# Performance work log

Hardware: AMD Instinct MI355X
Metric: run time of the kernel (lower is better)

## Reference

```python
import jax, jax.numpy as jnp
import numpy as np

B, S, D = 4, 1024, 2048
N_HEADS, N_KV_HEADS = 32, 8
HEAD_DIM = D // N_HEADS          # 64
HALF = HEAD_DIM // 2             # 32
N_REP = N_HEADS // N_KV_HEADS    # 4


def setup_inputs() -> dict:
    key = jax.random.key(0)
    ks = jax.random.split(key, 6)
    # rotary tables: freqs_cis = exp(i * t * theta^( -2j/d )), real cos/sin halves
    inv_freq = 1.0 / (10000.0 ** (np.arange(0, HEAD_DIM, 2, dtype=np.float32) / HEAD_DIM))
    t = np.arange(S, dtype=np.float32)
    angles = np.outer(t, inv_freq)  # [S, HALF]
    return {
        "x": jax.random.normal(ks[0], (B, S, D), dtype=jnp.float32),
        "pos_cos": jnp.asarray(np.cos(angles), dtype=jnp.float32),
        "pos_sin": jnp.asarray(np.sin(angles), dtype=jnp.float32),
        "wq": jax.random.normal(ks[1], (D, N_HEADS * HEAD_DIM), dtype=jnp.float32) / np.sqrt(D),
        "wk": jax.random.normal(ks[2], (D, N_KV_HEADS * HEAD_DIM), dtype=jnp.float32) / np.sqrt(D),
        "wv": jax.random.normal(ks[3], (D, N_KV_HEADS * HEAD_DIM), dtype=jnp.float32) / np.sqrt(D),
        "wo": jax.random.normal(ks[4], (D, D), dtype=jnp.float32) / np.sqrt(D),
    }


def _apply_rotary(t, cos, sin):
    # t: [B, S, H, head_dim]; pairs of consecutive elements form complex numbers
    te = t[..., 0::2]  # real parts  [B,S,H,HALF]
    to = t[..., 1::2]  # imag parts
    c = cos[None, :, None, :]
    s = sin[None, :, None, :]
    re = te * c - to * s
    im = te * s + to * c
    return jnp.stack([re, im], axis=-1).reshape(t.shape)


def reference(x, pos_cos, pos_sin, wq, wk, wv, wo):
    b, s, d = x.shape
    xq = (x @ wq).reshape(b, s, N_HEADS, HEAD_DIM)
    xk = (x @ wk).reshape(b, s, N_KV_HEADS, HEAD_DIM)
    xv = (x @ wv).reshape(b, s, N_KV_HEADS, HEAD_DIM)
    xq = _apply_rotary(xq, pos_cos, pos_sin)
    xk = _apply_rotary(xk, pos_cos, pos_sin)
    # GQA: repeat kv heads (kv head h -> heads h*N_REP..h*N_REP+N_REP-1)
    xk = jnp.repeat(xk, N_REP, axis=2)
    xv = jnp.repeat(xv, N_REP, axis=2)
    scores = jnp.einsum("bqhd,bkhd->bhqk", xq, xk) / np.sqrt(HEAD_DIM).astype(np.float32)
    causal = jnp.triu(jnp.ones((s, s), dtype=bool), k=1)
    scores = jnp.where(causal[None, None], jnp.float32(-jnp.inf), scores)
    attn = jax.nn.softmax(scores.astype(jnp.float32), axis=-1).astype(x.dtype)
    out = jnp.einsum("bhqk,bkhd->bqhd", attn, xv).reshape(b, s, d)
    return out @ wo
```

## Files before the change

### kernel.cpp

```cpp
#include <hip/hip_runtime.h>
#include <hip/hip_bf16.h>


typedef __bf16 bf16x8 __attribute__((ext_vector_type(8)));
typedef float  f32x4  __attribute__((ext_vector_type(4)));

#define DEV static __device__ __forceinline__

DEV unsigned short f2bf(float f) {
  __hip_bfloat16 h = __float2bfloat16(f);
  unsigned short u;
  __builtin_memcpy(&u, &h, 2);
  return u;
}
DEV float bf2f(unsigned short u) {
  unsigned int ui = ((unsigned int)u) << 16;
  float f;
  __builtin_memcpy(&f, &ui, 4);
  return f;
}

typedef const unsigned int __attribute__((address_space(1)))* as1_u32cp;
typedef unsigned int __attribute__((address_space(3)))* as3_u32p;

DEV void load16_lds(const unsigned short* g, unsigned short* l) {
  __builtin_amdgcn_global_load_lds((as1_u32cp)(unsigned long long)g,
                                   (as3_u32p)(unsigned int)(unsigned long long)l,
                                   16, 0, 0);
}

DEV f32x4 mfma16x16(bf16x8 a, bf16x8 b, f32x4 c) {
  return __builtin_amdgcn_mfma_f32_16x16x32_bf16(a, b, c, 0, 0, 0);
}

__global__ __launch_bounds__(256) void k_convert_x(const float* __restrict__ x,
                                                   unsigned short* __restrict__ xb, int n) {
  int i = (blockIdx.x * 256 + threadIdx.x) * 4;
  if (i < n) {
    float4 v = *(const float4*)(x + i);
    ushort4 o;
    o.x = f2bf(v.x); o.y = f2bf(v.y); o.z = f2bf(v.z); o.w = f2bf(v.w);
    *(ushort4*)(xb + i) = o;
  }
}

__global__ __launch_bounds__(256) void k_transpose_w(const float* __restrict__ src,
                                                     unsigned short* __restrict__ dst, int N) {
  __shared__ float t[32][33];
  const int n0 = blockIdx.x * 32, k0 = blockIdx.y * 32;
  const int tx = threadIdx.x & 31, ty = threadIdx.x >> 5;
#pragma unroll
  for (int i = 0; i < 4; i++) {
    int k = k0 + ty + i * 8;
    t[ty + i * 8][tx] = src[(size_t)k * N + n0 + tx];
  }
  __syncthreads();
#pragma unroll
  for (int i = 0; i < 4; i++) {
    int n = n0 + ty + i * 8;
    dst[(size_t)n * 2048 + k0 + tx] = f2bf(t[tx][ty + i * 8]);
  }
}

template <int OUTF32, int BN, int WM, int WN>
__global__ __launch_bounds__(512) void k_gemm8(const unsigned short* __restrict__ A,
                                               const unsigned short* __restrict__ Bt,
                                               void* __restrict__ Cp, int M, int N, int K) {
  constexpr int BM = 256;
  constexpr int FM = BM / WM / 16;
  constexpr int FN = BN / WN / 16;
  constexpr int LA = BM * 4 / 512;
  constexpr int LB = BN * 4 / 512;
  constexpr int LH = LA + LB;
  __shared__ __align__(16) unsigned short As[4][BM * 32];
  __shared__ __align__(16) unsigned short Bs[4][BN * 32];

  const int nbx = N / BN;
  const int nwg = gridDim.x;
  int wg = blockIdx.x;
  wg = (wg & 7) * (nwg >> 3) + (wg >> 3);
  const int bx = wg % nbx, by = wg / nbx;
  const int m0 = by << 8, n0 = bx * BN;
  const int tid = threadIdx.x;
  const int lane = tid & 63, wid = tid >> 6;
  const int wm = wid / WN, wn = wid % WN;
  const int l15 = lane & 15, kg = lane >> 4;
  const int H = K >> 5;
  const int NT = K >> 6;

  auto stageA = [&](int h, int i) {
    const int u = i * 512 + tid;
    const int row = u >> 2, sl = u & 3;
    const int gc = ((sl ^ ((row >> 1) & 3)) << 3);
    load16_lds(&A[(size_t)(m0 + row) * K + (h << 5) + gc],
               &As[h & 3][(i * 512 + (tid & ~63)) * 8]);
  };
  auto stageB = [&](int h, int i) {
    const int u = i * 512 + tid;
    const int row = u >> 2, sl = u & 3;
    const int gc = ((sl ^ ((row >> 1) & 3)) << 3);
    load16_lds(&Bt[(size_t)(n0 + row) * K + (h << 5) + gc],
               &Bs[h & 3][(i * 512 + (tid & ~63)) * 8]);
  };
  auto lda = [&](int s, int r) {
    return *(const bf16x8*)&As[s][r * 32 + ((kg ^ ((r >> 1) & 3)) << 3)];
  };
  auto ldb = [&](int s, int r) {
    return *(const bf16x8*)&Bs[s][r * 32 + ((kg ^ ((r >> 1) & 3)) << 3)];
  };

#define VMCNT_C2(c)                                                   \
  if ((c) == 2)      asm volatile("s_waitcnt vmcnt(%0)" ::"n"(2 * LH) : "memory"); \
  else if ((c) == 1) asm volatile("s_waitcnt vmcnt(%0)" ::"n"(LH) : "memory");     \
  else               asm volatile("s_waitcnt vmcnt(0)" ::: "memory");

  const int rowA0 = wm * (BM / WM) + l15;
  const int rowB0 = wn * (BN / WN) + l15;

  bf16x8 af[FM / 2], bf[FN];
  f32x4 acc[FM][FN] = {};

#pragma unroll
  for (int h = 0; h < 3; h++) {
    stageA(h, 0); stageA(h, 1);
    stageB(h, 0); if (LB > 1) stageB(h, 1);
  }
  asm volatile("s_waitcnt vmcnt(%0)" ::"n"(2 * LH) : "memory");
  __builtin_amdgcn_s_barrier();

  for (int t = 0; t < NT; t++) {
    const int s0 = (2 * t) & 3, s1 = (2 * t + 1) & 3;
    const int h3 = 2 * t + 3, h4 = 2 * t + 4;
    const bool v2 = (2 * t + 2) < H, v3 = h3 < H, v4 = h4 < H;

#pragma unroll
    for (int f = 0; f < FM / 2; f++) af[f] = lda(s0, rowA0 + f * 16);
#pragma unroll
    for (int g = 0; g < FN; g++) bf[g] = ldb(s0, rowB0 + g * 16);
    if (v3) { stageA(h3, 0); stageA(h3, 1); }
    __builtin_amdgcn_s_barrier();
    __builtin_amdgcn_s_setprio(1);
#pragma unroll
    for (int f = 0; f < FM / 2; f++)
#pragma unroll
      for (int g = 0; g < FN; g++) acc[f][g] = mfma16x16(af[f], bf[g], acc[f][g]);
    __builtin_amdgcn_s_setprio(0);

#pragma unroll
    for (int f = 0; f < FM / 2; f++) af[f] = lda(s0, rowA0 + (FM / 2 + f) * 16);
    if (v3) { stageB(h3, 0); if (LB > 1) stageB(h3, 1); }
    __builtin_amdgcn_s_barrier();
    __builtin_amdgcn_s_setprio(1);
#pragma unroll
    for (int f = 0; f < FM / 2; f++)
#pragma unroll
      for (int g = 0; g < FN; g++)
        acc[FM / 2 + f][g] = mfma16x16(af[f], bf[g], acc[FM / 2 + f][g]);
    __builtin_amdgcn_s_setprio(0);
    { const int c = (int)v2 + (int)v3; VMCNT_C2(c) }
    __builtin_amdgcn_s_barrier();

#pragma unroll
    for (int f = 0; f < FM / 2; f++) af[f] = lda(s1, rowA0 + f * 16);
#pragma unroll
    for (int g = 0; g < FN; g++) bf[g] = ldb(s1, rowB0 + g * 16);
    if (v4) { stageA(h4, 0); stageA(h4, 1); }
    __builtin_amdgcn_s_barrier();
    __builtin_amdgcn_s_setprio(1);
#pragma unroll
    for (int f = 0; f < FM / 2; f++)
#pragma unroll
      for (int g = 0; g < FN; g++) acc[f][g] = mfma16x16(af[f], bf[g], acc[f][g]);
    __builtin_amdgcn_s_setprio(0);

#pragma unroll
    for (int f = 0; f < FM / 2; f++) af[f] = lda(s1, rowA0 + (FM / 2 + f) * 16);
    if (v4) { stageB(h4, 0); if (LB > 1) stageB(h4, 1); }
    __builtin_amdgcn_s_barrier();
    __builtin_amdgcn_s_setprio(1);
#pragma unroll
    for (int f = 0; f < FM / 2; f++)
#pragma unroll
      for (int g = 0; g < FN; g++)
        acc[FM / 2 + f][g] = mfma16x16(af[f], bf[g], acc[FM / 2 + f][g]);
    __builtin_amdgcn_s_setprio(0);
    { const int c = (int)v3 + (int)v4; VMCNT_C2(c) }
    __builtin_amdgcn_s_barrier();
  }
#undef VMCNT_C2

  const int orow = m0 + wm * (BM / WM) + kg * 4;
#pragma unroll
  for (int fm = 0; fm < FM; fm++) {
#pragma unroll
    for (int fn = 0; fn < FN; fn++) {
      const int col = n0 + wn * (BN / WN) + fn * 16 + l15;
#pragma unroll
      for (int j = 0; j < 4; j++) {
        const size_t off = (size_t)(orow + fm * 16 + j) * N + col;
        if (OUTF32)
          ((float*)Cp)[off] = acc[fm][fn][j];
        else
          ((unsigned short*)Cp)[off] = f2bf(acc[fm][fn][j]);
      }
    }
  }
}

__global__ __launch_bounds__(256) void k_rope(unsigned short* __restrict__ qkv,
                                              const float* __restrict__ ctab,
                                              const float* __restrict__ stab) {
  const int idx = blockIdx.x * 256 + threadIdx.x;
  const int row = idx / 1280;
  const int r = idx - row * 1280;
  const int head = r >> 5, pair = r & 31;
  const int s = row & 1023;
  const int col = (head < 32) ? (head * 64 + pair * 2) : (2048 + (head - 32) * 64 + pair * 2);
  const float c = ctab[s * 32 + pair], sn = stab[s * 32 + pair];
  const size_t base = (size_t)row * 3072 + col;
  const float e = bf2f(qkv[base]), o = bf2f(qkv[base + 1]);
  qkv[base]     = f2bf(e * c - o * sn);
  qkv[base + 1] = f2bf(e * sn + o * c);
}

__global__ __launch_bounds__(256) void k_vt(const unsigned short* __restrict__ qkv,
                                            unsigned short* __restrict__ vt) {
  __shared__ unsigned short t[32][33];
  const int st0 = blockIdx.x * 32;
  const int d0 = blockIdx.y * 32;
  const int bkh = blockIdx.z;
  const int b = bkh >> 3, kh = bkh & 7;
  const int tx = threadIdx.x & 31, ty = threadIdx.x >> 5;
#pragma unroll
  for (int i = 0; i < 4; i++) {
    int s = st0 + ty + i * 8;
    t[ty + i * 8][tx] = qkv[(size_t)(b * 1024 + s) * 3072 + 2560 + kh * 64 + d0 + tx];
  }
  __syncthreads();
#pragma unroll
  for (int i = 0; i < 4; i++) {
    int d = d0 + ty + i * 8;
    vt[(size_t)(bkh * 64 + d) * 1024 + st0 + tx] = t[tx][ty + i * 8];
  }
}

__global__ __launch_bounds__(256) void k_attn(const unsigned short* __restrict__ qkv,
                                              const unsigned short* __restrict__ vt,
                                              unsigned short* __restrict__ ao) {
  __shared__ __align__(16) unsigned short Ks[2][64 * 64];
  __shared__ __align__(16) unsigned short Vs[2][64 * 64];
  __shared__ __align__(16) unsigned short P[4][16][72];

  const int bid = blockIdx.x;
  const int qt = 15 - (bid >> 7);
  const int hb = bid & 127;
  const int h = hb & 31, b = hb >> 5;
  const int q0 = qt << 6;
  const int wid = threadIdx.x >> 6, lane = threadIdx.x & 63;
  const int l15 = lane & 15, kg = lane >> 4;
  const int kh = h >> 2;
  const int qbase = b * 1024 + q0 + wid * 16;
  const int nt = qt + 1;
  const float NEGINF = -__builtin_inff();

  bf16x8 aq0, aq1;
  {
    const size_t qoff = (size_t)(qbase + l15) * 3072 + h * 64 + kg * 8;
    aq0 = *(const bf16x8*)&qkv[qoff];
    aq1 = *(const bf16x8*)&qkv[qoff + 32];
#pragma unroll
    for (int i = 0; i < 8; i++) {
      aq0[i] = (__bf16)((float)aq0[i] * 0.18033688011112042f);
      aq1[i] = (__bf16)((float)aq1[i] * 0.18033688011112042f);
    }
  }

  const int l8 = lane >> 3;
  const int colel = ((lane & 7) ^ l8) * 8;
  const size_t krowbase = (size_t)(b * 1024) * 3072 + 2048 + kh * 64 + colel;
  const size_t vrowbase = (size_t)((b * 8 + kh) * 64) * 1024 + colel;

#pragma unroll
  for (int i = 0; i < 2; i++) {
    const int r = wid * 16 + i * 8 + l8;
    load16_lds(&qkv[krowbase + (size_t)r * 3072], &Ks[0][(wid * 16 + i * 8) * 64]);
    load16_lds(&vt[vrowbase + (size_t)r * 1024], &Vs[0][(wid * 16 + i * 8) * 64]);
  }
  asm volatile("s_waitcnt vmcnt(0)" ::: "memory");
  __builtin_amdgcn_s_barrier();

  f32x4 o[4] = {};
  float mrow[4] = {NEGINF, NEGINF, NEGINF, NEGINF};
  float lrow[4] = {0.f, 0.f, 0.f, 0.f};

  const int swz = (l15 & 7) * 8;

  for (int t = 0; t < nt; t++) {
    const int cur = t & 1;
    if (t + 1 < nt) {
      const size_t kv1 = (size_t)((t + 1) << 6);
#pragma unroll
      for (int i = 0; i < 2; i++) {
        const int r = wid * 16 + i * 8 + l8;
        load16_lds(&qkv[krowbase + (kv1 + r) * 3072], &Ks[cur ^ 1][(wid * 16 + i * 8) * 64]);
        load16_lds(&vt[vrowbase + (size_t)r * 1024 + kv1], &Vs[cur ^ 1][(wid * 16 + i * 8) * 64]);
      }
    }
    const int kv0 = t << 6;

    f32x4 sc[4] = {};
    __builtin_amdgcn_s_setprio(1);
#pragma unroll
    for (int ct = 0; ct < 4; ct++) {
      const unsigned short* kr = &Ks[cur][(ct * 16 + l15) * 64];
      bf16x8 bk0 = *(const bf16x8*)&kr[(kg * 8) ^ swz];
      bf16x8 bk1 = *(const bf16x8*)&kr[(kg * 8 + 32) ^ swz];
      sc[ct] = mfma16x16(aq0, bk0, sc[ct]);
      sc[ct] = mfma16x16(aq1, bk1, sc[ct]);
    }
    __builtin_amdgcn_s_setprio(0);

    float p[4][4];
    if (t == qt) {
#pragma unroll
      for (int reg = 0; reg < 4; reg++) {
        const int rowg = q0 + wid * 16 + kg * 4 + reg;
#pragma unroll
        for (int ct = 0; ct < 4; ct++) {
          const int colg = kv0 + ct * 16 + l15;
          p[ct][reg] = (colg > rowg) ? NEGINF : sc[ct][reg];
        }
      }
    } else {
#pragma unroll
      for (int reg = 0; reg < 4; reg++)
#pragma unroll
        for (int ct = 0; ct < 4; ct++) p[ct][reg] = sc[ct][reg];
    }

    float rm[4];
#pragma unroll
    for (int reg = 0; reg < 4; reg++) {
      float v = fmaxf(fmaxf(p[0][reg], p[1][reg]), fmaxf(p[2][reg], p[3][reg]));
#pragma unroll
      for (int off = 1; off < 16; off <<= 1) v = fmaxf(v, __shfl_xor(v, off));
      rm[reg] = v;
    }

    const int okl = (rm[0] <= mrow[0] + 8.f) && (rm[1] <= mrow[1] + 8.f) &&
                    (rm[2] <= mrow[2] + 8.f) && (rm[3] <= mrow[3] + 8.f);
    if (__all(okl)) {
#pragma unroll
      for (int reg = 0; reg < 4; reg++) {
        float rs = 0.f;
#pragma unroll
        for (int ct = 0; ct < 4; ct++) {
          const float e = exp2f(p[ct][reg] - mrow[reg]);
          p[ct][reg] = e;
          rs += e;
        }
#pragma unroll
        for (int off = 1; off < 16; off <<= 1) rs += __shfl_xor(rs, off);
        lrow[reg] += rs;
      }
    } else {
      float fac[4];
#pragma unroll
      for (int reg = 0; reg < 4; reg++) {
        const float mnew = fmaxf(mrow[reg], rm[reg]);
        fac[reg] = exp2f(mrow[reg] - mnew);
        float rs = 0.f;
#pragma unroll
        for (int ct = 0; ct < 4; ct++) {
          const float e = exp2f(p[ct][reg] - mnew);
          p[ct][reg] = e;
          rs += e;
        }
#pragma unroll
        for (int off = 1; off < 16; off <<= 1) rs += __shfl_xor(rs, off);
        lrow[reg] = lrow[reg] * fac[reg] + rs;
        mrow[reg] = mnew;
      }
#pragma unroll
      for (int ct = 0; ct < 4; ct++) {
        o[ct][0] *= fac[0]; o[ct][1] *= fac[1]; o[ct][2] *= fac[2]; o[ct][3] *= fac[3];
      }
    }

#pragma unroll
    for (int reg = 0; reg < 4; reg++)
#pragma unroll
      for (int ct = 0; ct < 4; ct++)
        P[wid][kg * 4 + reg][ct * 16 + l15] = f2bf(p[ct][reg]);

    bf16x8 ap0 = *(const bf16x8*)&P[wid][l15][kg * 8];
    bf16x8 ap1 = *(const bf16x8*)&P[wid][l15][32 + kg * 8];

    __builtin_amdgcn_s_setprio(1);
#pragma unroll
    for (int ct = 0; ct < 4; ct++) {
      const unsigned short* vr = &Vs[cur][(ct * 16 + l15) * 64];
      bf16x8 bv0 = *(const bf16x8*)&vr[(kg * 8) ^ swz];
      bf16x8 bv1 = *(const bf16x8*)&vr[(kg * 8 + 32) ^ swz];
      o[ct] = mfma16x16(ap0, bv0, o[ct]);
      o[ct] = mfma16x16(ap1, bv1, o[ct]);
    }
    __builtin_amdgcn_s_setprio(0);

    asm volatile("s_waitcnt vmcnt(0)" ::: "memory");
    __builtin_amdgcn_s_barrier();
  }

#pragma unroll
  for (int ct = 0; ct < 4; ct++) {
#pragma unroll
    for (int reg = 0; reg < 4; reg++) {
      const float val = o[ct][reg] / lrow[reg];
      ao[(size_t)(qbase + kg * 4 + reg) * 2048 + h * 64 + ct * 16 + l15] = f2bf(val);
    }
  }
}

extern "C" void kernel_launch(void* const* d_in, const int* in_sizes, int n_in,
                              void* d_out, int out_size, void* d_ws, size_t ws_size,
                              hipStream_t stream) {
  const float* x    = (const float*)d_in[0];
  const float* pcos = (const float*)d_in[1];
  const float* psin = (const float*)d_in[2];
  const float* wq   = (const float*)d_in[3];
  const float* wk   = (const float*)d_in[4];
  const float* wv   = (const float*)d_in[5];
  const float* wo   = (const float*)d_in[6];

  char* ws = (char*)d_ws;
  unsigned short* XB  = (unsigned short*)(ws);
  unsigned short* WT  = (unsigned short*)(ws + 16777216);
  unsigned short* WOT = (unsigned short*)(ws + 29360128);
  unsigned short* QKV = (unsigned short*)(ws + 37748736);
  unsigned short* VT  = (unsigned short*)(ws + 62914560);

  k_convert_x<<<8192, 256, 0, stream>>>(x, XB, 8388608);
  k_transpose_w<<<dim3(64, 64), 256, 0, stream>>>(wq, WT, 2048);
  k_transpose_w<<<dim3(16, 64), 256, 0, stream>>>(wk, WT + (size_t)2048 * 2048, 512);
  k_transpose_w<<<dim3(16, 64), 256, 0, stream>>>(wv, WT + (size_t)2560 * 2048, 512);
  k_transpose_w<<<dim3(64, 64), 256, 0, stream>>>(wo, WOT, 2048);

  k_gemm8<0, 256, 2, 4><<<192, 512, 0, stream>>>(XB, WT, QKV, 4096, 3072, 2048);
  k_rope<<<20480, 256, 0, stream>>>(QKV, pcos, psin);
  k_vt<<<dim3(32, 2, 32), 256, 0, stream>>>(QKV, VT);
  k_attn<<<2048, 256, 0, stream>>>(QKV, VT, XB);
  k_gemm8<1, 128, 4, 2><<<256, 512, 0, stream>>>(XB, WOT, d_out, 4096, 2048, 2048);
}
```

Baseline: 302.3 us.

## Transpose attention MFMA layout so each lane owns one query row; vectorize RoPE

The QK^T and PV MFMAs swap their operands so the score tile is transposed, and each lane then holds a single query row. Row max and row sum need only two cross-lane shuffles instead of four-step reductions over four rows, and the lazy-rescale branch is dropped in favour of an unconditional single-row rescale. P is written to LDS as packed ushort4 with an XOR swizzle, and the output is stored as ushort4. RoPE is rewritten so each thread handles 8 bf16 elements with vector loads and stores and float4 tables, which cuts the thread count and the number of memory transactions. Removing the lazy-rescale branch adds an unconditional multiply on the accumulators every iteration.

New measurement: 277.9 us. 8.1% less time.

```diff
diff --git a/kernel.cpp b/kernel.cpp
--- a/kernel.cpp
+++ b/kernel.cpp
@@ -4,6 +4,7 @@
 
 typedef __bf16 bf16x8 __attribute__((ext_vector_type(8)));
 typedef float  f32x4  __attribute__((ext_vector_type(4)));
+typedef unsigned short u16x8 __attribute__((ext_vector_type(8)));
 
 #define DEV static __device__ __forceinline__
 
@@ -211,16 +212,24 @@
                                               const float* __restrict__ ctab,
                                               const float* __restrict__ stab) {
   const int idx = blockIdx.x * 256 + threadIdx.x;
-  const int row = idx / 1280;
-  const int r = idx - row * 1280;
-  const int head = r >> 5, pair = r & 31;
+  const int row = idx / 320;
+  const int r = idx - row * 320;
+  const int head = r >> 3, quad = r & 7;
   const int s = row & 1023;
-  const int col = (head < 32) ? (head * 64 + pair * 2) : (2048 + (head - 32) * 64 + pair * 2);
-  const float c = ctab[s * 32 + pair], sn = stab[s * 32 + pair];
+  const int col = ((head < 32) ? head * 64 : 2048 + (head - 32) * 64) + quad * 8;
+  const float4 c = *(const float4*)&ctab[s * 32 + quad * 4];
+  const float4 sn = *(const float4*)&stab[s * 32 + quad * 4];
   const size_t base = (size_t)row * 3072 + col;
-  const float e = bf2f(qkv[base]), o = bf2f(qkv[base + 1]);
-  qkv[base]     = f2bf(e * c - o * sn);
-  qkv[base + 1] = f2bf(e * sn + o * c);
+  u16x8 v = *(const u16x8*)&qkv[base];
+  const float cc[4] = {c.x, c.y, c.z, c.w};
+  const float ss[4] = {sn.x, sn.y, sn.z, sn.w};
+#pragma unroll
+  for (int i = 0; i < 4; i++) {
+    const float e = bf2f(v[2 * i]), o = bf2f(v[2 * i + 1]);
+    v[2 * i]     = f2bf(e * cc[i] - o * ss[i]);
+    v[2 * i + 1] = f2bf(e * ss[i] + o * cc[i]);
+  }
+  *(u16x8*)&qkv[base] = v;
 }
 
 __global__ __launch_bounds__(256) void k_vt(const unsigned short* __restrict__ qkv,
@@ -249,7 +258,7 @@
                                               unsigned short* __restrict__ ao) {
   __shared__ __align__(16) unsigned short Ks[2][64 * 64];
   __shared__ __align__(16) unsigned short Vs[2][64 * 64];
-  __shared__ __align__(16) unsigned short P[4][16][72];
+  __shared__ __align__(16) unsigned short P[4][16][64];
 
   const int bid = blockIdx.x;
   const int qt = 15 - (bid >> 7);
@@ -290,10 +299,11 @@
   __builtin_amdgcn_s_barrier();
 
   f32x4 o[4] = {};
-  float mrow[4] = {NEGINF, NEGINF, NEGINF, NEGINF};
-  float lrow[4] = {0.f, 0.f, 0.f, 0.f};
+  float mrow = NEGINF;
+  float lrow = 0.f;
 
   const int swz = (l15 & 7) * 8;
+  const int psw = (l15 & 7) * 8;
 
   for (int t = 0; t < nt; t++) {
     const int cur = t & 1;
@@ -306,7 +316,6 @@
         load16_lds(&vt[vrowbase + (size_t)r * 1024 + kv1], &Vs[cur ^ 1][(wid * 16 + i * 8) * 64]);
       }
     }
-    const int kv0 = t << 6;
 
     f32x4 sc[4] = {};
     __builtin_amdgcn_s_setprio(1);
@@ -315,86 +324,65 @@
       const unsigned short* kr = &Ks[cur][(ct * 16 + l15) * 64];
       bf16x8 bk0 = *(const bf16x8*)&kr[(kg * 8) ^ swz];
       bf16x8 bk1 = *(const bf16x8*)&kr[(kg * 8 + 32) ^ swz];
-      sc[ct] = mfma16x16(aq0, bk0, sc[ct]);
-      sc[ct] = mfma16x16(aq1, bk1, sc[ct]);
+      sc[ct] = mfma16x16(bk0, aq0, sc[ct]);
+      sc[ct] = mfma16x16(bk1, aq1, sc[ct]);
     }
     __builtin_amdgcn_s_setprio(0);
 
     float p[4][4];
     if (t == qt) {
+      const int qloc = wid * 16 + l15;
+#pragma unroll
+      for (int ct = 0; ct < 4; ct++)
+#pragma unroll
+        for (int reg = 0; reg < 4; reg++) {
+          const int kloc = ct * 16 + kg * 4 + reg;
+          p[ct][reg] = (kloc > qloc) ? NEGINF : sc[ct][reg];
+        }
+    } else {
+#pragma unroll
+      for (int ct = 0; ct < 4; ct++)
+#pragma unroll
+        for (int reg = 0; reg < 4; reg++) p[ct][reg] = sc[ct][reg];
+    }
+
+    float rm = NEGINF;
+#pragma unroll
+    for (int ct = 0; ct < 4; ct++)
+      rm = fmaxf(rm, fmaxf(fmaxf(p[ct][0], p[ct][1]), fmaxf(p[ct][2], p[ct][3])));
+    rm = fmaxf(rm, __shfl_xor(rm, 16));
+    rm = fmaxf(rm, __shfl_xor(rm, 32));
+
+    const float mnew = fmaxf(mrow, rm);
+    const float fac = exp2f(mrow - mnew);
+    float rs = 0.f;
+#pragma unroll
+    for (int ct = 0; ct < 4; ct++)
 #pragma unroll
       for (int reg = 0; reg < 4; reg++) {
-        const int rowg = q0 + wid * 16 + kg * 4 + reg;
-#pragma unroll
-        for (int ct = 0; ct < 4; ct++) {
-          const int colg = kv0 + ct * 16 + l15;
-          p[ct][reg] = (colg > rowg) ? NEGINF : sc[ct][reg];
-        }
+        const float e = exp2f(p[ct][reg] - mnew);
+        p[ct][reg] = e;
+        rs += e;
       }
-    } else {
-#pragma unroll
-      for (int reg = 0; reg < 4; reg++)
-#pragma unroll
-        for (int ct = 0; ct < 4; ct++) p[ct][reg] = sc[ct][reg];
-    }
-
-    float rm[4];
-#pragma unroll
-    for (int reg = 0; reg < 4; reg++) {
-      float v = fmaxf(fmaxf(p[0][reg], p[1][reg]), fmaxf(p[2][reg], p[3][reg]));
-#pragma unroll
-      for (int off = 1; off < 16; off <<= 1) v = fmaxf(v, __shfl_xor(v, off));
-      rm[reg] = v;
-    }
-
-    const int okl = (rm[0] <= mrow[0] + 8.f) && (rm[1] <= mrow[1] + 8.f) &&
-                    (rm[2] <= mrow[2] + 8.f) && (rm[3] <= mrow[3] + 8.f);
-    if (__all(okl)) {
-#pragma unroll
-      for (int reg = 0; reg < 4; reg++) {
-        float rs = 0.f;
-#pragma unroll
-        for (int ct = 0; ct < 4; ct++) {
-          const float e = exp2f(p[ct][reg] - mrow[reg]);
-          p[ct][reg] = e;
-          rs += e;
-        }
-#pragma unroll
-        for (int off = 1; off < 16; off <<= 1) rs += __shfl_xor(rs, off);
-        lrow[reg] += rs;
-      }
-    } else {
-      float fac[4];
-#pragma unroll
-      for (int reg = 0; reg < 4; reg++) {
-        const float mnew = fmaxf(mrow[reg], rm[reg]);
-        fac[reg] = exp2f(mrow[reg] - mnew);
-        float rs = 0.f;
-#pragma unroll
-        for (int ct = 0; ct < 4; ct++) {
-          const float e = exp2f(p[ct][reg] - mnew);
-          p[ct][reg] = e;
-          rs += e;
-        }
-#pragma unroll
-        for (int off = 1; off < 16; off <<= 1) rs += __shfl_xor(rs, off);
-        lrow[reg] = lrow[reg] * fac[reg] + rs;
-        mrow[reg] = mnew;
-      }
-#pragma unroll
-      for (int ct = 0; ct < 4; ct++) {
-        o[ct][0] *= fac[0]; o[ct][1] *= fac[1]; o[ct][2] *= fac[2]; o[ct][3] *= fac[3];
-      }
-    }
-
-#pragma unroll
-    for (int reg = 0; reg < 4; reg++)
-#pragma unroll
-      for (int ct = 0; ct < 4; ct++)
-        P[wid][kg * 4 + reg][ct * 16 + l15] = f2bf(p[ct][reg]);
-
-    bf16x8 ap0 = *(const bf16x8*)&P[wid][l15][kg * 8];
-    bf16x8 ap1 = *(const bf16x8*)&P[wid][l15][32 + kg * 8];
+    rs += __shfl_xor(rs, 16);
+    rs += __shfl_xor(rs, 32);
+    lrow = lrow * fac + rs;
+    mrow = mnew;
+#pragma unroll
+    for (int ct = 0; ct < 4; ct++) {
+      o[ct][0] *= fac; o[ct][1] *= fac; o[ct][2] *= fac; o[ct][3] *= fac;
+    }
+
+#pragma unroll
+    for (int ct = 0; ct < 4; ct++) {
+      ushort4 pk;
+      pk.x = f2bf(p[ct][0]); pk.y = f2bf(p[ct][1]);
+      pk.z = f2bf(p[ct][2]); pk.w = f2bf(p[ct][3]);
+      *(ushort4*)&P[wid][l15][(ct * 16 + kg * 4) ^ psw] = pk;
+    }
+
+    bf16x8 ap0 = *(const bf16x8*)&P[wid][l15][(kg * 8) ^ psw];
+    bf16x8 ap1 = *(const bf16x8*)&P[wid][l15][(32 + kg * 8) ^ psw];
 
     __builtin_amdgcn_s_setprio(1);
 #pragma unroll
@@ -402,8 +390,8 @@
       const unsigned short* vr = &Vs[cur][(ct * 16 + l15) * 64];
       bf16x8 bv0 = *(const bf16x8*)&vr[(kg * 8) ^ swz];
       bf16x8 bv1 = *(const bf16x8*)&vr[(kg * 8 + 32) ^ swz];
-      o[ct] = mfma16x16(ap0, bv0, o[ct]);
-      o[ct] = mfma16x16(ap1, bv1, o[ct]);
+      o[ct] = mfma16x16(bv0, ap0, o[ct]);
+      o[ct] = mfma16x16(bv1, ap1, o[ct]);
     }
     __builtin_amdgcn_s_setprio(0);
 
@@ -411,13 +399,14 @@
     __builtin_amdgcn_s_barrier();
   }
 
+  const float rl = 1.0f / lrow;
+  const size_t obase = (size_t)(qbase + l15) * 2048 + h * 64;
 #pragma unroll
   for (int ct = 0; ct < 4; ct++) {
-#pragma unroll
-    for (int reg = 0; reg < 4; reg++) {
-      const float val = o[ct][reg] / lrow[reg];
-      ao[(size_t)(qbase + kg * 4 + reg) * 2048 + h * 64 + ct * 16 + l15] = f2bf(val);
-    }
+    ushort4 ov;
+    ov.x = f2bf(o[ct][0] * rl); ov.y = f2bf(o[ct][1] * rl);
+    ov.z = f2bf(o[ct][2] * rl); ov.w = f2bf(o[ct][3] * rl);
+    *(ushort4*)&ao[obase + ct * 16 + kg * 4] = ov;
   }
 }
 
@@ -446,7 +435,7 @@
   k_transpose_w<<<dim3(64, 64), 256, 0, stream>>>(wo, WOT, 2048);
 
   k_gemm8<0, 256, 2, 4><<<192, 512, 0, stream>>>(XB, WT, QKV, 4096, 3072, 2048);
-  k_rope<<<20480, 256, 0, stream>>>(QKV, pcos, psin);
+  k_rope<<<5120, 256, 0, stream>>>(QKV, pcos, psin);
   k_vt<<<dim3(32, 2, 32), 256, 0, stream>>>(QKV, VT);
   k_attn<<<2048, 256, 0, stream>>>(QKV, VT, XB);
   k_gemm8<1, 128, 4, 2><<<256, 512, 0, stream>>>(XB, WOT, d_out, 4096, 2048, 2048);
```
